# Kernel tuning notes

Hardware: AMD Instinct MI355X
Metric: run time of the kernel (lower is better)

The kernel has to match this reference:

```python
import jax, jax.numpy as jnp
import numpy as np
import math

M = 0.2
S = 30.0
COS_M = math.cos(M)
SIN_M = math.sin(M)
TH = math.cos(math.pi - M)
MM = math.sin(math.pi - M) * M


def setup_inputs() -> dict:
    key = jax.random.key(0)
    k1, k2, k3 = jax.random.split(key, 3)
    B, D, C = 1024, 192, 100000
    x = jax.random.normal(k1, (B, D), dtype=jnp.float32)
    weight = jax.random.normal(k2, (C, D), dtype=jnp.float32)
    label = jax.random.randint(k3, (B,), 0, C, dtype=jnp.int64)
    return {"x": x, "weight": weight, "label": label}


def _l2norm(v, axis=-1, eps=1e-12):
    # matches F.normalize(p=2): v / max(||v||, eps)
    n = jnp.sqrt(jnp.sum(v * v, axis=axis, keepdims=True))
    return v / jnp.maximum(n, eps)


def reference(x, weight, label):
    B = x.shape[0]
    cosine = _l2norm(x) @ _l2norm(weight).T            # [B, C]
    sine = jnp.sqrt(jnp.clip(1.0 - cosine * cosine, 0.0, 1.0))
    phi = cosine * COS_M - sine * SIN_M
    phi = jnp.where(cosine - TH > 0, phi, cosine - MM)
    one_hot = jax.nn.one_hot(label, cosine.shape[1], dtype=cosine.dtype)
    output = (one_hot * phi + (1.0 - one_hot) * cosine) * S
    # cross entropy (mean reduction)
    logp = jax.nn.log_softmax(output, axis=-1)
    loss = -jnp.mean(jnp.take_along_axis(logp, label[:, None], axis=1)[:, 0])
    # top-1 accuracy (percent), detached metric
    pred = jnp.argmax(output, axis=-1)
    prec1 = jnp.mean((pred == label).astype(jnp.float32)) * 100.0
    return loss, prec1
```

## Files before the change

### kernel.cpp

```cpp
#include <hip/hip_runtime.h>
#include <math.h>

#define B_ROWS   1024
#define DIM      192
#define NCLS     100000
#define S_SCALE  30.0f
#define COS_M    0.98006657784124163f
#define SIN_M    0.19866933079506122f
#define TH_C     (-0.98006657784124163f)
#define MM_C     0.039733866159012243f
#define L2E30    43.2808512266689f

#define NTILE_B  784
#define NCHUNKR  16
#define ASEG_CH  1536
#define NSLOT    1568

#define NCHUNKC  1568
#define CSPLIT   128
#define NSLOT2   128
#define PACK_WGRID 3136
#define PACK_GRID  3168

typedef float floatx4 __attribute__((ext_vector_type(4)));
typedef __bf16 bf16x8 __attribute__((ext_vector_type(8)));

__device__ __forceinline__ unsigned int f2bf(float x) {
    unsigned int u = __float_as_uint(x);
    u = (u + 0x7fffu + ((u >> 16) & 1u)) >> 16;
    return u;
}
__device__ __forceinline__ unsigned int pack2(float lo, float hi) {
    return f2bf(lo) | (f2bf(hi) << 16);
}
__device__ __forceinline__ float fexp2(float x) {
#if __has_builtin(__builtin_amdgcn_exp2f)
    return __builtin_amdgcn_exp2f(x);
#else
    float r; __asm__("v_exp_f32 %0, %1" : "=v"(r) : "v"(x)); return r;
#endif
}
template <int N>
__device__ __forceinline__ float ror16(float x) {
    return __int_as_float(__builtin_amdgcn_mov_dpp(
        __float_as_int(x), 0x120 | N, 0xF, 0xF, false));
}


__global__ __launch_bounds__(256)
void pack_kernel(const float* __restrict__ x, const float* __restrict__ w,
                 unsigned short* __restrict__ asw, unsigned short* __restrict__ wsw,
                 float* __restrict__ accum)
{
    const int bid = blockIdx.x;
    const int t = threadIdx.x;
    const int r = t >> 3, oct = t & 7;

    const float* src;
    unsigned short* dst;
    int row;
    bool live;
    if (bid < PACK_WGRID) {
        row = bid * 32 + r;  live = (row < NCLS);  src = w;  dst = wsw;
    } else {
        row = (bid - PACK_WGRID) * 32 + r;  live = true;  src = x;  dst = asw;
        if (bid == PACK_WGRID && t < 4) accum[t] = 0.0f;
    }

    float4 buf[6];
    float s = 0.f;
    if (live) {
        const float4* sp = (const float4*)(src + (size_t)row * DIM) + oct * 6;
        #pragma unroll
        for (int q = 0; q < 6; ++q) {
            float4 v = sp[q];
            buf[q] = v;
            s += v.x * v.x + v.y * v.y + v.z * v.z + v.w * v.w;
        }
    } else {
        #pragma unroll
        for (int q = 0; q < 6; ++q) buf[q] = make_float4(0.f, 0.f, 0.f, 0.f);
    }
    s += __shfl_xor(s, 1);
    s += __shfl_xor(s, 2);
    s += __shfl_xor(s, 4);
    const float inv = live ? (1.0f / fmaxf(sqrtf(s), 1e-12f)) : 0.0f;

    const int cc = row >> 6, c64 = row & 63;
    #pragma unroll
    for (int j = 0; j < 3; ++j) {
        const int k8 = oct * 3 + j;
        uint4 o;
        float4 a0 = buf[2 * j], a1 = buf[2 * j + 1];
        o.x = pack2(a0.x * inv, a0.y * inv);
        o.y = pack2(a0.z * inv, a0.w * inv);
        o.z = pack2(a1.x * inv, a1.y * inv);
        o.w = pack2(a1.z * inv, a1.w * inv);
        *(uint4*)(dst + ((size_t)(cc * 24 + k8) * 64 + c64) * 8) = o;
    }
}

__global__ __launch_bounds__(256, 2)
void gemm_stats4_kernel(const unsigned short* __restrict__ asw,
                        const unsigned short* __restrict__ wsw,
                        float2* __restrict__ pslot)
{
    const int bid  = blockIdx.x;
    const int cs   = bid & 127;
    const int rb   = bid >> 7;
    const int tid  = threadIdx.x;
    const int wv   = tid >> 6;
    const int lane = tid & 63;
    const int quad = lane >> 4, mrow = lane & 15;

    bf16x8 xfr[4][6];
    {
        const unsigned short* ab = asw + (size_t)(rb * 4 + wv) * (24 * 64 * 8);
        #pragma unroll
        for (int a = 0; a < 4; ++a)
            #pragma unroll
            for (int ks = 0; ks < 6; ++ks)
                xfr[a][ks] = *(const bf16x8*)(ab +
                    (size_t)((ks * 4 + quad) * 64 + a * 16 + mrow) * 8);
    }

    const int nch   = 12 + (cs < 32 ? 1 : 0);
    const int cbase = cs * 12 + (cs < 32 ? cs : 32);
    const unsigned short* wp = wsw + (size_t)cbase * 12288
                             + quad * 512 + mrow * 8;

    float s_acc[4][4];
    float m_acc[4][4];
    #pragma unroll
    for (int a = 0; a < 4; ++a)
        #pragma unroll
        for (int r = 0; r < 4; ++r) { s_acc[a][r] = 0.f; m_acc[a][r] = -1e30f; }

    bf16x8 b0[4], b1[4];
    #pragma unroll
    for (int ni = 0; ni < 4; ++ni) {
        b0[ni] = *(const bf16x8*)(wp + ni * 128);
        b1[ni] = *(const bf16x8*)(wp + 2048 + ni * 128);
    }

    #pragma unroll 1
    for (int c = 0; c < nch; ++c, wp += 12288) {
        floatx4 acc[4][4];
        #pragma unroll
        for (int a = 0; a < 4; ++a)
            #pragma unroll
            for (int ni = 0; ni < 4; ++ni) {
                floatx4 z = {0.f, 0.f, 0.f, 0.f};
                acc[a][ni] = z;
            }
        #pragma unroll
        for (int ks = 0; ks < 6; ++ks) {
            const unsigned short* np = wp + (size_t)(ks + 2) * 2048;
            bf16x8 n0 = *(const bf16x8*)(np);
            bf16x8 n1 = *(const bf16x8*)(np + 128);
            bf16x8 n2 = *(const bf16x8*)(np + 256);
            bf16x8 n3 = *(const bf16x8*)(np + 384);
            __builtin_amdgcn_s_setprio(1);
            #pragma unroll
            for (int a = 0; a < 4; ++a) {
                acc[a][0] = __builtin_amdgcn_mfma_f32_16x16x32_bf16(
                    xfr[a][ks], b0[0], acc[a][0], 0, 0, 0);
                acc[a][1] = __builtin_amdgcn_mfma_f32_16x16x32_bf16(
                    xfr[a][ks], b0[1], acc[a][1], 0, 0, 0);
                acc[a][2] = __builtin_amdgcn_mfma_f32_16x16x32_bf16(
                    xfr[a][ks], b0[2], acc[a][2], 0, 0, 0);
                acc[a][3] = __builtin_amdgcn_mfma_f32_16x16x32_bf16(
                    xfr[a][ks], b0[3], acc[a][3], 0, 0, 0);
            }
            __builtin_amdgcn_s_setprio(0);
            b0[0] = b1[0]; b0[1] = b1[1]; b0[2] = b1[2]; b0[3] = b1[3];
            b1[0] = n0;    b1[1] = n1;    b1[2] = n2;    b1[3] = n3;
        }
        #pragma unroll
        for (int a = 0; a < 4; ++a)
            #pragma unroll
            for (int r = 0; r < 4; ++r) {
                float v0 = acc[a][0][r], v1 = acc[a][1][r];
                float v2 = acc[a][2][r], v3 = acc[a][3][r];
                m_acc[a][r] = fmaxf(fmaxf(fmaxf(fmaxf(v0, v1), v2), v3),
                                    m_acc[a][r]);
                s_acc[a][r] += (fexp2(fmaf(v0, L2E30, -L2E30))
                              + fexp2(fmaf(v1, L2E30, -L2E30)))
                             + (fexp2(fmaf(v2, L2E30, -L2E30))
                              + fexp2(fmaf(v3, L2E30, -L2E30)));
            }
    }

    const int rowb = rb * 256 + wv * 64;
    #pragma unroll
    for (int a = 0; a < 4; ++a)
        #pragma unroll
        for (int r = 0; r < 4; ++r) {
            float s = s_acc[a][r], m = m_acc[a][r];
            s += ror16<1>(s); s += ror16<2>(s); s += ror16<4>(s); s += ror16<8>(s);
            m = fmaxf(m, ror16<1>(m)); m = fmaxf(m, ror16<2>(m));
            m = fmaxf(m, ror16<4>(m)); m = fmaxf(m, ror16<8>(m));
            if (mrow == 0)
                pslot[(size_t)cs * B_ROWS + rowb + a * 16 + quad * 4 + r] =
                    make_float2(m, s);
        }
}

__global__ __launch_bounds__(256)
void finalize2_kernel(const float2* __restrict__ pslot,
                      const float* __restrict__ x, const float* __restrict__ w,
                      const int* __restrict__ label,
                      float* __restrict__ accum, float* __restrict__ out)
{
    __shared__ float2 red[8][32];
    const int t = threadIdx.x, rr = t & 31, g = t >> 5;
    {
        const int row = blockIdx.x * 32 + rr;
        float M = -1e30f, L = 0.f;
        #pragma unroll
        for (int s = 0; s < NSLOT2 / 8; ++s) {
            float2 p = pslot[(size_t)(s * 8 + g) * B_ROWS + row];
            M = fmaxf(M, p.x);
            L += p.y;
        }
        red[g][rr] = make_float2(M, L);
    }
    __syncthreads();
    if (t < 32) {
        const int row = blockIdx.x * 32 + t;
        float Mc = -1e30f, L = 0.f;
        #pragma unroll
        for (int g2 = 0; g2 < 8; ++g2) {
            float2 p = red[g2][t];
            Mc = fmaxf(Mc, p.x);
            L += p.y;
        }

        const int lab = label[row];
        const float4* xr = (const float4*)(x + (size_t)row * DIM);
        const float4* wr = (const float4*)(w + (size_t)lab * DIM);
        float dot = 0.f, nx = 0.f, nw = 0.f;
        #pragma unroll
        for (int q = 0; q < 48; ++q) {
            float4 a = xr[q], b = wr[q];
            dot += a.x * b.x + a.y * b.y + a.z * b.z + a.w * b.w;
            nx  += a.x * a.x + a.y * a.y + a.z * a.z + a.w * a.w;
            nw  += b.x * b.x + b.y * b.y + b.z * b.z + b.w * b.w;
        }
        float cosl    = dot / fmaxf(sqrtf(nx) * sqrtf(nw), 1e-12f);
        float t_plain = S_SCALE * cosl;
        float sine    = sqrtf(fmaxf(0.f, fminf(1.f, 1.f - cosl * cosl)));
        float phi     = cosl * COS_M - sine * SIN_M;
        float modv    = ((cosl - TH_C) > 0.f) ? phi : (cosl - MM_C);
        float t_mod   = S_SCALE * modv;

        float Ladj = L - __expf(t_plain - 30.0f) + __expf(t_mod - 30.0f);
        Ladj = fmaxf(Ladj, 1e-37f);
        float loss = (30.0f + logf(Ladj)) - t_mod;
        float corr = (t_mod > S_SCALE * Mc) ? 1.f : 0.f;

        #pragma unroll
        for (int off = 16; off > 0; off >>= 1) {
            loss += __shfl_xor(loss, off);
            corr += __shfl_xor(corr, off);
        }
        if (t == 0) {
            atomicAdd(&accum[0], loss);
            atomicAdd(&accum[1], corr);
            __threadfence();
            int old = atomicAdd((int*)accum + 2, 1);
            if (old == (int)gridDim.x - 1) {
                float a0 = atomicAdd(&accum[0], 0.0f);
                float a1 = atomicAdd(&accum[1], 0.0f);
                out[0] = a0 * (1.0f / (float)B_ROWS);
                out[1] = a1 * (100.0f / (float)B_ROWS);
            }
        }
    }
}


__global__ __launch_bounds__(256)
void prep_kernel(const float* __restrict__ x, unsigned short* __restrict__ asw,
                 float* __restrict__ accum)
{
    const int ab = blockIdx.x;
    const int t = threadIdx.x;
    if (ab == 0 && t < 4) accum[t] = 0.0f;
    const int r = t >> 1, half = t & 1;
    const int row = ab * 128 + r;
    const int c = ab * 2 + (r >> 6);
    const int r64 = r & 63;

    float4 buf[24];
    float s = 0.f;
    const float4* sp = (const float4*)(x + (size_t)row * DIM) + half * 24;
    #pragma unroll
    for (int q = 0; q < 24; ++q) {
        float4 v = sp[q];
        buf[q] = v;
        s += v.x * v.x + v.y * v.y + v.z * v.z + v.w * v.w;
    }
    s += __shfl_xor(s, 1);
    const float inv = 1.0f / fmaxf(sqrtf(s), 1e-12f);
    #pragma unroll
    for (int j = 0; j < 12; ++j) {
        const int k8 = half * 12 + j;
        uint4 o;
        float4 a0 = buf[2 * j], a1 = buf[2 * j + 1];
        o.x = pack2(a0.x * inv, a0.y * inv);
        o.y = pack2(a0.z * inv, a0.w * inv);
        o.z = pack2(a1.x * inv, a1.y * inv);
        o.w = pack2(a1.z * inv, a1.w * inv);
        *(uint4*)(asw + ((size_t)c * ASEG_CH + k8 * 64 + r64) * 8) = o;
    }
}

__global__ __launch_bounds__(256, 3)
void gemm_stats_kernel(const float* __restrict__ w,
                       const unsigned short* __restrict__ asw,
                       unsigned int* __restrict__ pslot)
{
    __shared__ __align__(16) char lds[49152];
    const int tid  = threadIdx.x;
    const int wave = tid >> 6;
    const int lane = tid & 63;
    const int quad = lane >> 4;
    const int mrow = lane & 15;
    const int rg   = wave >> 1;
    const int cgr  = wave & 1;

    {
        const int r = tid >> 1, half = tid & 1;
        const int col = blockIdx.x * 128 + r;
        const bool live = (col < NCLS);
        float4 buf[24];
        float s = 0.f;
        if (live) {
            const float4* sp = (const float4*)(w + (size_t)col * DIM) + half * 24;
            #pragma unroll
            for (int q = 0; q < 24; ++q) {
                float4 v = sp[q];
                buf[q] = v;
                s += v.x * v.x + v.y * v.y + v.z * v.z + v.w * v.w;
            }
        }
        s += __shfl_xor(s, 1);
        const float inv = live ? (1.0f / fmaxf(sqrtf(s), 1e-12f)) : 0.0f;
        #pragma unroll
        for (int j = 0; j < 12; ++j) {
            const int k8 = half * 12 + j;
            uint4 o = make_uint4(0u, 0u, 0u, 0u);
            if (live) {
                float4 a0 = buf[2 * j], a1 = buf[2 * j + 1];
                o.x = pack2(a0.x * inv, a0.y * inv);
                o.y = pack2(a0.z * inv, a0.w * inv);
                o.z = pack2(a1.x * inv, a1.y * inv);
                o.w = pack2(a1.z * inv, a1.w * inv);
            }
            *(uint4*)(lds + (size_t)(k8 * 128 + r) * 16) = o;
        }
    }
    __syncthreads();

    bf16x8 bfr[6][4];
    #pragma unroll
    for (int ks = 0; ks < 6; ++ks)
        #pragma unroll
        for (int ni = 0; ni < 4; ++ni)
            bfr[ks][ni] = *(const bf16x8*)(lds +
                (((ks * 4 + quad) * 128) + cgr * 64 + ni * 16 + mrow) * 16);

    const int slot = blockIdx.x * 2 + cgr;
    #pragma unroll 2
    for (int c = 0; c < NCHUNKR; ++c) {
        const unsigned short* ab = asw + (size_t)c * ASEG_CH * 8;
        floatx4 acc[2][4];
        #pragma unroll
        for (int mi = 0; mi < 2; ++mi)
            #pragma unroll
            for (int ni = 0; ni < 4; ++ni) {
                floatx4 z = {0.f, 0.f, 0.f, 0.f};
                acc[mi][ni] = z;
            }
        #pragma unroll
        for (int ks = 0; ks < 6; ++ks) {
            bf16x8 a0 = *(const bf16x8*)(ab +
                (size_t)(((ks * 4 + quad) * 64) + rg * 32 + mrow) * 8);
            bf16x8 a1 = *(const bf16x8*)(ab +
                (size_t)(((ks * 4 + quad) * 64) + rg * 32 + 16 + mrow) * 8);
            #pragma unroll
            for (int ni = 0; ni < 4; ++ni)
                acc[0][ni] = __builtin_amdgcn_mfma_f32_16x16x32_bf16(
                    a0, bfr[ks][ni], acc[0][ni], 0, 0, 0);
            #pragma unroll
            for (int ni = 0; ni < 4; ++ni)
                acc[1][ni] = __builtin_amdgcn_mfma_f32_16x16x32_bf16(
                    a1, bfr[ks][ni], acc[1][ni], 0, 0, 0);
        }

        #pragma unroll
        for (int mi = 0; mi < 2; ++mi)
            #pragma unroll
            for (int r = 0; r < 4; ++r) {
                float v0 = acc[mi][0][r], v1 = acc[mi][1][r];
                float v2 = acc[mi][2][r], v3 = acc[mi][3][r];
                float m = fmaxf(fmaxf(v0, v1), fmaxf(v2, v3));
                float s = fexp2(fmaf(v0, L2E30, -L2E30))
                        + fexp2(fmaf(v1, L2E30, -L2E30))
                        + fexp2(fmaf(v2, L2E30, -L2E30))
                        + fexp2(fmaf(v3, L2E30, -L2E30));
                s += ror16<1>(s); s += ror16<2>(s);
                s += ror16<4>(s); s += ror16<8>(s);
                m = fmaxf(m, ror16<1>(m)); m = fmaxf(m, ror16<2>(m));
                m = fmaxf(m, ror16<4>(m)); m = fmaxf(m, ror16<8>(m));
                if (mrow == mi * 4 + r)
                    pslot[(size_t)slot * B_ROWS +
                          c * 64 + rg * 32 + mi * 16 + quad * 4 + r] = pack2(m, s);
            }
    }
}

__global__ __launch_bounds__(256)
void finalize_kernel(const unsigned int* __restrict__ pslot,
                     const float* __restrict__ x, const float* __restrict__ w,
                     const int* __restrict__ label,
                     float* __restrict__ accum, float* __restrict__ out)
{
    __shared__ float2 red[8][32];
    const int t = threadIdx.x, rr = t & 31, g = t >> 5;
    {
        const int row = blockIdx.x * 32 + rr;
        float M = -1e30f, L = 0.f;
        for (int s = g; s < NSLOT; s += 8) {
            unsigned int u = pslot[(size_t)s * B_ROWS + row];
            M = fmaxf(M, __uint_as_float(u << 16));
            L += __uint_as_float(u & 0xFFFF0000u);
        }
        red[g][rr] = make_float2(M, L);
    }
    __syncthreads();
    if (t < 32) {
        const int row = blockIdx.x * 32 + t;
        float Mc = -1e30f, L = 0.f;
        #pragma unroll
        for (int g2 = 0; g2 < 8; ++g2) {
            float2 p = red[g2][t];
            Mc = fmaxf(Mc, p.x);
            L += p.y;
        }

        const int lab = label[row];
        const float4* xr = (const float4*)(x + (size_t)row * DIM);
        const float4* wr = (const float4*)(w + (size_t)lab * DIM);
        float dot = 0.f, nx = 0.f, nw = 0.f;
        #pragma unroll
        for (int q = 0; q < 48; ++q) {
            float4 a = xr[q], b = wr[q];
            dot += a.x * b.x + a.y * b.y + a.z * b.z + a.w * b.w;
            nx  += a.x * a.x + a.y * a.y + a.z * a.z + a.w * a.w;
            nw  += b.x * b.x + b.y * b.y + b.z * b.z + b.w * b.w;
        }
        float cosl    = dot / fmaxf(sqrtf(nx) * sqrtf(nw), 1e-12f);
        float t_plain = S_SCALE * cosl;
        float sine    = sqrtf(fmaxf(0.f, fminf(1.f, 1.f - cosl * cosl)));
        float phi     = cosl * COS_M - sine * SIN_M;
        float modv    = ((cosl - TH_C) > 0.f) ? phi : (cosl - MM_C);
        float t_mod   = S_SCALE * modv;

        float Ladj = L - __expf(t_plain - 30.0f) + __expf(t_mod - 30.0f);
        Ladj = fmaxf(Ladj, 1e-37f);
        float loss = (30.0f + logf(Ladj)) - t_mod;
        float corr = (t_mod > S_SCALE * Mc) ? 1.f : 0.f;

        #pragma unroll
        for (int off = 16; off > 0; off >>= 1) {
            loss += __shfl_xor(loss, off);
            corr += __shfl_xor(corr, off);
        }
        if (t == 0) {
            atomicAdd(&accum[0], loss);
            atomicAdd(&accum[1], corr);
            __threadfence();
            int old = atomicAdd((int*)accum + 2, 1);
            if (old == (int)gridDim.x - 1) {
                float a0 = atomicAdd(&accum[0], 0.0f);
                float a1 = atomicAdd(&accum[1], 0.0f);
                out[0] = a0 * (1.0f / (float)B_ROWS);
                out[1] = a1 * (100.0f / (float)B_ROWS);
            }
        }
    }
}

extern "C" void kernel_launch(void* const* d_in, const int* in_sizes, int n_in,
                              void* d_out, int out_size, void* d_ws, size_t ws_size,
                              hipStream_t stream)
{
    const float* x     = (const float*)d_in[0];
    const float* w     = (const float*)d_in[1];
    const int*   label = (const int*)d_in[2];
    float* out = (float*)d_out;

    char* ws = (char*)d_ws;
    float* accum = (float*)ws;
    unsigned short* asw = (unsigned short*)(ws + 256);
    const size_t asw_bytes = (size_t)NCHUNKR * ASEG_CH * 16;

    const size_t wsw_bytes    = (size_t)NCHUNKC * 24 * 64 * 16;
    const size_t pslot2_bytes = (size_t)NSLOT2 * B_ROWS * 8;
    const size_t need_new = 256 + asw_bytes + wsw_bytes + pslot2_bytes;

    if (ws_size >= need_new) {
        unsigned short* wsw = (unsigned short*)(ws + 256 + asw_bytes);
        float2* pslot2 = (float2*)(ws + 256 + asw_bytes + wsw_bytes);
        pack_kernel<<<dim3(PACK_GRID), dim3(256), 0, stream>>>(x, w, asw, wsw, accum);
        gemm_stats4_kernel<<<dim3(4 * CSPLIT), dim3(256), 0, stream>>>(asw, wsw, pslot2);
        finalize2_kernel<<<dim3(B_ROWS / 32), dim3(256), 0, stream>>>(
            pslot2, x, w, label, accum, out);
    } else {
        unsigned int* pslot = (unsigned int*)(ws + 256 + asw_bytes);
        prep_kernel<<<dim3(8), dim3(256), 0, stream>>>(x, asw, accum);
        gemm_stats_kernel<<<dim3(NTILE_B), dim3(256), 0, stream>>>(w, asw, pslot);
        finalize_kernel<<<dim3(B_ROWS / 32), dim3(256), 0, stream>>>(
            pslot, x, w, label, accum, out);
    }
}
```

Baseline: 168.5 us.

## Switch GEMM to 32x32x16 MFMA and fold log2e*30 scale into packed x

Replaces the 16x16x32 MFMA tiling with 32x32x16 MFMAs over two 32-row tiles per wave, with a 4-deep rotating register prefetch of weight fragments. The softmax scale (30*log2e) is folded into the x normalization during packing, so the epilogue feeds accumulators straight into exp2 and drops the per-element FMA. Finalize rescales the sum by exp(-30) and converts the max back from log2 units. Folding the scale into bf16 x changes rounding slightly, and without the -30 offset the exp2 sums may get large, though they stay within fp32 range.

```diff
diff --git a/kernel.cpp b/kernel.cpp
--- a/kernel.cpp
+++ b/kernel.cpp
@@ -10,6 +10,8 @@
 #define TH_C     (-0.98006657784124163f)
 #define MM_C     0.039733866159012243f
 #define L2E30    43.2808512266689f
+#define EXPM30   9.357622968840175e-14f
+#define LN2_C    0.69314718055994531f
 
 #define NTILE_B  784
 #define NCHUNKR  16
@@ -22,7 +24,8 @@
 #define PACK_WGRID 3136
 #define PACK_GRID  3168
 
-typedef float floatx4 __attribute__((ext_vector_type(4)));
+typedef float floatx4  __attribute__((ext_vector_type(4)));
+typedef float floatx16 __attribute__((ext_vector_type(16)));
 typedef __bf16 bf16x8 __attribute__((ext_vector_type(8)));
 
 __device__ __forceinline__ unsigned int f2bf(float x) {
@@ -60,10 +63,11 @@
     unsigned short* dst;
     int row;
     bool live;
+    bool isx;
     if (bid < PACK_WGRID) {
-        row = bid * 32 + r;  live = (row < NCLS);  src = w;  dst = wsw;
+        row = bid * 32 + r;  live = (row < NCLS);  src = w;  dst = wsw;  isx = false;
     } else {
-        row = (bid - PACK_WGRID) * 32 + r;  live = true;  src = x;  dst = asw;
+        row = (bid - PACK_WGRID) * 32 + r;  live = true;  src = x;  dst = asw;  isx = true;
         if (bid == PACK_WGRID && t < 4) accum[t] = 0.0f;
     }
 
@@ -84,7 +88,8 @@
     s += __shfl_xor(s, 1);
     s += __shfl_xor(s, 2);
     s += __shfl_xor(s, 4);
-    const float inv = live ? (1.0f / fmaxf(sqrtf(s), 1e-12f)) : 0.0f;
+    float inv = live ? (1.0f / fmaxf(sqrtf(s), 1e-12f)) : 0.0f;
+    if (isx) inv *= L2E30;
 
     const int cc = row >> 6, c64 = row & 63;
     #pragma unroll
@@ -100,8 +105,14 @@
     }
 }
 
+__device__ __forceinline__ constexpr int poff(int q) {
+    return (q < 12) ? q * 1024
+         : (q < 24) ? 256 + (q - 12) * 1024
+                    : 12288 + (q - 24) * 1024;
+}
+
 __global__ __launch_bounds__(256, 2)
-void gemm_stats4_kernel(const unsigned short* __restrict__ asw,
+void gemm_stats5_kernel(const unsigned short* __restrict__ asw,
                         const unsigned short* __restrict__ wsw,
                         float2* __restrict__ pslot)
 {
@@ -111,98 +122,91 @@
     const int tid  = threadIdx.x;
     const int wv   = tid >> 6;
     const int lane = tid & 63;
-    const int quad = lane >> 4, mrow = lane & 15;
-
-    bf16x8 xfr[4][6];
+    const int col  = lane & 31;
+    const int kh   = lane >> 5;
+
+    bf16x8 xfr[2][12];
     {
-        const unsigned short* ab = asw + (size_t)(rb * 4 + wv) * (24 * 64 * 8);
-        #pragma unroll
-        for (int a = 0; a < 4; ++a)
+        const unsigned short* al = asw + (size_t)(rb * 4 + wv) * 12288
+                                 + kh * 512 + col * 8;
+        #pragma unroll
+        for (int t = 0; t < 2; ++t)
             #pragma unroll
-            for (int ks = 0; ks < 6; ++ks)
-                xfr[a][ks] = *(const bf16x8*)(ab +
-                    (size_t)((ks * 4 + quad) * 64 + a * 16 + mrow) * 8);
+            for (int ks = 0; ks < 12; ++ks)
+                xfr[t][ks] = *(const bf16x8*)(al + ks * 1024 + t * 256);
     }
 
     const int nch   = 12 + (cs < 32 ? 1 : 0);
     const int cbase = cs * 12 + (cs < 32 ? cs : 32);
     const unsigned short* wp = wsw + (size_t)cbase * 12288
-                             + quad * 512 + mrow * 8;
-
-    float s_acc[4][4];
-    float m_acc[4][4];
-    #pragma unroll
-    for (int a = 0; a < 4; ++a)
-        #pragma unroll
-        for (int r = 0; r < 4; ++r) { s_acc[a][r] = 0.f; m_acc[a][r] = -1e30f; }
-
-    bf16x8 b0[4], b1[4];
-    #pragma unroll
-    for (int ni = 0; ni < 4; ++ni) {
-        b0[ni] = *(const bf16x8*)(wp + ni * 128);
-        b1[ni] = *(const bf16x8*)(wp + 2048 + ni * 128);
-    }
+                             + kh * 512 + col * 8;
+
+    float s_acc[2][16];
+    float m_acc[2][16];
+    #pragma unroll
+    for (int t = 0; t < 2; ++t)
+        #pragma unroll
+        for (int r = 0; r < 16; ++r) { s_acc[t][r] = 0.f; m_acc[t][r] = -1e30f; }
+
+    bf16x8 bL[4];
+    #pragma unroll
+    for (int i = 0; i < 4; ++i)
+        bL[i] = *(const bf16x8*)(wp + poff(i));
 
     #pragma unroll 1
     for (int c = 0; c < nch; ++c, wp += 12288) {
-        floatx4 acc[4][4];
-        #pragma unroll
-        for (int a = 0; a < 4; ++a)
-            #pragma unroll
-            for (int ni = 0; ni < 4; ++ni) {
-                floatx4 z = {0.f, 0.f, 0.f, 0.f};
-                acc[a][ni] = z;
-            }
-        #pragma unroll
-        for (int ks = 0; ks < 6; ++ks) {
-            const unsigned short* np = wp + (size_t)(ks + 2) * 2048;
-            bf16x8 n0 = *(const bf16x8*)(np);
-            bf16x8 n1 = *(const bf16x8*)(np + 128);
-            bf16x8 n2 = *(const bf16x8*)(np + 256);
-            bf16x8 n3 = *(const bf16x8*)(np + 384);
-            __builtin_amdgcn_s_setprio(1);
-            #pragma unroll
-            for (int a = 0; a < 4; ++a) {
-                acc[a][0] = __builtin_amdgcn_mfma_f32_16x16x32_bf16(
-                    xfr[a][ks], b0[0], acc[a][0], 0, 0, 0);
-                acc[a][1] = __builtin_amdgcn_mfma_f32_16x16x32_bf16(
-                    xfr[a][ks], b0[1], acc[a][1], 0, 0, 0);
-                acc[a][2] = __builtin_amdgcn_mfma_f32_16x16x32_bf16(
-                    xfr[a][ks], b0[2], acc[a][2], 0, 0, 0);
-                acc[a][3] = __builtin_amdgcn_mfma_f32_16x16x32_bf16(
-                    xfr[a][ks], b0[3], acc[a][3], 0, 0, 0);
-            }
-            __builtin_amdgcn_s_setprio(0);
-            b0[0] = b1[0]; b0[1] = b1[1]; b0[2] = b1[2]; b0[3] = b1[3];
-            b1[0] = n0;    b1[1] = n1;    b1[2] = n2;    b1[3] = n3;
-        }
-        #pragma unroll
-        for (int a = 0; a < 4; ++a)
-            #pragma unroll
-            for (int r = 0; r < 4; ++r) {
-                float v0 = acc[a][0][r], v1 = acc[a][1][r];
-                float v2 = acc[a][2][r], v3 = acc[a][3][r];
-                m_acc[a][r] = fmaxf(fmaxf(fmaxf(fmaxf(v0, v1), v2), v3),
-                                    m_acc[a][r]);
-                s_acc[a][r] += (fexp2(fmaf(v0, L2E30, -L2E30))
-                              + fexp2(fmaf(v1, L2E30, -L2E30)))
-                             + (fexp2(fmaf(v2, L2E30, -L2E30))
-                              + fexp2(fmaf(v3, L2E30, -L2E30)));
-            }
+        floatx16 accA, accB;
+        #pragma unroll
+        for (int r = 0; r < 16; ++r) { accA[r] = 0.f; accB[r] = 0.f; }
+        #pragma unroll
+        for (int p = 0; p < 12; ++p) {
+            bf16x8 bf = bL[p & 3];
+            bL[p & 3] = *(const bf16x8*)(wp + poff(p + 4));
+            accA = __builtin_amdgcn_mfma_f32_32x32x16_bf16(xfr[0][p], bf, accA, 0, 0, 0);
+            accB = __builtin_amdgcn_mfma_f32_32x32x16_bf16(xfr[1][p], bf, accB, 0, 0, 0);
+        }
+        #pragma unroll
+        for (int r = 0; r < 16; ++r) {
+            float vA = accA[r], vB = accB[r];
+            m_acc[0][r] = fmaxf(m_acc[0][r], vA);
+            m_acc[1][r] = fmaxf(m_acc[1][r], vB);
+            s_acc[0][r] += fexp2(vA);
+            s_acc[1][r] += fexp2(vB);
+        }
+        #pragma unroll
+        for (int r = 0; r < 16; ++r) { accA[r] = 0.f; accB[r] = 0.f; }
+        #pragma unroll
+        for (int p = 12; p < 24; ++p) {
+            bf16x8 bf = bL[p & 3];
+            bL[p & 3] = *(const bf16x8*)(wp + poff(p + 4));
+            accA = __builtin_amdgcn_mfma_f32_32x32x16_bf16(xfr[0][p - 12], bf, accA, 0, 0, 0);
+            accB = __builtin_amdgcn_mfma_f32_32x32x16_bf16(xfr[1][p - 12], bf, accB, 0, 0, 0);
+        }
+        #pragma unroll
+        for (int r = 0; r < 16; ++r) {
+            float vA = accA[r], vB = accB[r];
+            m_acc[0][r] = fmaxf(m_acc[0][r], vA);
+            m_acc[1][r] = fmaxf(m_acc[1][r], vB);
+            s_acc[0][r] += fexp2(vA);
+            s_acc[1][r] += fexp2(vB);
+        }
     }
 
     const int rowb = rb * 256 + wv * 64;
     #pragma unroll
-    for (int a = 0; a < 4; ++a)
-        #pragma unroll
-        for (int r = 0; r < 4; ++r) {
-            float s = s_acc[a][r], m = m_acc[a][r];
+    for (int t = 0; t < 2; ++t)
+        #pragma unroll
+        for (int r = 0; r < 16; ++r) {
+            float s = s_acc[t][r], m = m_acc[t][r];
             s += ror16<1>(s); s += ror16<2>(s); s += ror16<4>(s); s += ror16<8>(s);
+            s += __shfl_xor(s, 16);
             m = fmaxf(m, ror16<1>(m)); m = fmaxf(m, ror16<2>(m));
             m = fmaxf(m, ror16<4>(m)); m = fmaxf(m, ror16<8>(m));
-            if (mrow == 0)
-                pslot[(size_t)cs * B_ROWS + rowb + a * 16 + quad * 4 + r] =
-                    make_float2(m, s);
+            m = fmaxf(m, __shfl_xor(m, 16));
+            if (col == 0) {
+                const int rl = (r & 3) + 8 * (r >> 2) + 4 * kh + t * 32;
+                pslot[(size_t)cs * B_ROWS + rowb + rl] = make_float2(m, s);
+            }
         }
 }
 
@@ -254,10 +258,10 @@
         float modv    = ((cosl - TH_C) > 0.f) ? phi : (cosl - MM_C);
         float t_mod   = S_SCALE * modv;
 
-        float Ladj = L - __expf(t_plain - 30.0f) + __expf(t_mod - 30.0f);
+        float Ladj = L * EXPM30 - __expf(t_plain - 30.0f) + __expf(t_mod - 30.0f);
         Ladj = fmaxf(Ladj, 1e-37f);
         float loss = (30.0f + logf(Ladj)) - t_mod;
-        float corr = (t_mod > S_SCALE * Mc) ? 1.f : 0.f;
+        float corr = (t_mod > Mc * LN2_C) ? 1.f : 0.f;
 
         #pragma unroll
         for (int off = 16; off > 0; off >>= 1) {
@@ -515,7 +519,7 @@
         unsigned short* wsw = (unsigned short*)(ws + 256 + asw_bytes);
         float2* pslot2 = (float2*)(ws + 256 + asw_bytes + wsw_bytes);
         pack_kernel<<<dim3(PACK_GRID), dim3(256), 0, stream>>>(x, w, asw, wsw, accum);
-        gemm_stats4_kernel<<<dim3(4 * CSPLIT), dim3(256), 0, stream>>>(asw, wsw, pslot2);
+        gemm_stats5_kernel<<<dim3(4 * CSPLIT), dim3(256), 0, stream>>>(asw, wsw, pslot2);
         finalize2_kernel<<<dim3(B_ROWS / 32), dim3(256), 0, stream>>>(
             pslot2, x, w, label, accum, out);
     } else {
```

Result: slower. 174.7 us (+3.7%).

## Stage weight tiles through double-buffered LDS and fold exp scale into packed activations

Applied to the files above, without the earlier changes.

The GEMM kernel now loads each weight chunk into a double-buffered LDS region with a register-staged prefetch of the next chunk, replacing the per-wave direct global register double buffer. The pack kernel writes through LDS for coalesced stores, reorders its block-to-chunk mapping to follow the GEMM consumer order, and pre-multiplies normalized x by log2(e)*30 so the softmax exp needs no per-element FMA. Finalize rescales the sum and the max comparison to match. This adds a barrier per chunk and LDS traffic, and increases bf16 rounding exposure on the scaled activations.

```diff
diff --git a/kernel.cpp b/kernel.cpp
--- a/kernel.cpp
+++ b/kernel.cpp
@@ -10,6 +10,8 @@
 #define TH_C     (-0.98006657784124163f)
 #define MM_C     0.039733866159012243f
 #define L2E30    43.2808512266689f
+#define EXPM30   9.357622968840175e-14f
+#define LN2_C    0.69314718055994531f
 
 #define NTILE_B  784
 #define NCHUNKR  16
@@ -48,25 +50,43 @@
 
 
 __global__ __launch_bounds__(256)
-void pack_kernel(const float* __restrict__ x, const float* __restrict__ w,
-                 unsigned short* __restrict__ asw, unsigned short* __restrict__ wsw,
-                 float* __restrict__ accum)
-{
+void pack2_kernel(const float* __restrict__ x, const float* __restrict__ w,
+                  unsigned short* __restrict__ asw, unsigned short* __restrict__ wsw,
+                  float* __restrict__ accum)
+{
+    __shared__ uint4 lds_pk[32][25];
     const int bid = blockIdx.x;
     const int t = threadIdx.x;
     const int r = t >> 3, oct = t & 7;
 
     const float* src;
-    unsigned short* dst;
-    int row;
-    bool live;
+    unsigned short* dstc;
+    int rowbase, half;
+    bool wside;
     if (bid < PACK_WGRID) {
-        row = bid * 32 + r;  live = (row < NCLS);  src = w;  dst = wsw;
+        const int k = bid & 7, j = bid >> 3;
+        int cs, cc, h;
+        if (j < 104) {
+            const int i = j / 26; h = j % 26;
+            cs = k + 8 * i;  cc = cs * 13 + (h >> 1);
+        } else {
+            const int j2 = j - 104;
+            const int i = 4 + j2 / 24; h = j2 % 24;
+            cs = k + 8 * i;  cc = 416 + (cs - 32) * 12 + (h >> 1);
+        }
+        half = h & 1;
+        rowbase = cc * 64 + half * 32;
+        src = w;  dstc = wsw + (size_t)cc * 12288;  wside = true;
     } else {
-        row = (bid - PACK_WGRID) * 32 + r;  live = true;  src = x;  dst = asw;
+        const int xb = bid - PACK_WGRID;
+        half = xb & 1;
+        rowbase = xb * 32;
+        src = x;  dstc = asw + (size_t)(xb >> 1) * 12288;  wside = false;
         if (bid == PACK_WGRID && t < 4) accum[t] = 0.0f;
     }
 
+    const int row = rowbase + r;
+    const bool live = !wside || (row < NCLS);
     float4 buf[6];
     float s = 0.f;
     if (live) {
@@ -84,9 +104,9 @@
     s += __shfl_xor(s, 1);
     s += __shfl_xor(s, 2);
     s += __shfl_xor(s, 4);
-    const float inv = live ? (1.0f / fmaxf(sqrtf(s), 1e-12f)) : 0.0f;
-
-    const int cc = row >> 6, c64 = row & 63;
+    float inv = live ? (1.0f / fmaxf(sqrtf(s), 1e-12f)) : 0.0f;
+    if (!wside) inv *= L2E30;
+
     #pragma unroll
     for (int j = 0; j < 3; ++j) {
         const int k8 = oct * 3 + j;
@@ -96,15 +116,24 @@
         o.y = pack2(a0.z * inv, a0.w * inv);
         o.z = pack2(a1.x * inv, a1.y * inv);
         o.w = pack2(a1.z * inv, a1.w * inv);
-        *(uint4*)(dst + ((size_t)(cc * 24 + k8) * 64 + c64) * 8) = o;
+        lds_pk[r][k8] = o;
+    }
+    __syncthreads();
+    #pragma unroll
+    for (int j = 0; j < 3; ++j) {
+        const int flat = j * 256 + t;
+        const int sseg = flat >> 5, rr = flat & 31;
+        *(uint4*)(dstc + ((size_t)(sseg * 64) + half * 32 + rr) * 8)
+            = lds_pk[rr][sseg];
     }
 }
 
 __global__ __launch_bounds__(256, 2)
-void gemm_stats4_kernel(const unsigned short* __restrict__ asw,
+void gemm_stats7_kernel(const unsigned short* __restrict__ asw,
                         const unsigned short* __restrict__ wsw,
                         float2* __restrict__ pslot)
 {
+    __shared__ __align__(16) char lds[49152];
     const int bid  = blockIdx.x;
     const int cs   = bid & 127;
     const int rb   = bid >> 7;
@@ -115,7 +144,7 @@
 
     bf16x8 xfr[4][6];
     {
-        const unsigned short* ab = asw + (size_t)(rb * 4 + wv) * (24 * 64 * 8);
+        const unsigned short* ab = asw + (size_t)(rb * 4 + wv) * 12288;
         #pragma unroll
         for (int a = 0; a < 4; ++a)
             #pragma unroll
@@ -124,10 +153,9 @@
                     (size_t)((ks * 4 + quad) * 64 + a * 16 + mrow) * 8);
     }
 
-    const int nch   = 12 + (cs < 32 ? 1 : 0);
-    const int cbase = cs * 12 + (cs < 32 ? cs : 32);
-    const unsigned short* wp = wsw + (size_t)cbase * 12288
-                             + quad * 512 + mrow * 8;
+    const int nch = 12 + (cs < 32 ? 1 : 0);
+    const char* wp0 = (const char*)(wsw
+                    + (size_t)(cs * 12 + (cs < 32 ? cs : 32)) * 12288);
 
     float s_acc[4][4];
     float m_acc[4][4];
@@ -136,15 +164,32 @@
         #pragma unroll
         for (int r = 0; r < 4; ++r) { s_acc[a][r] = 0.f; m_acc[a][r] = -1e30f; }
 
-    bf16x8 b0[4], b1[4];
-    #pragma unroll
-    for (int ni = 0; ni < 4; ++ni) {
-        b0[ni] = *(const bf16x8*)(wp + ni * 128);
-        b1[ni] = *(const bf16x8*)(wp + 2048 + ni * 128);
-    }
+    const int soff = wv * 6144 + lane * 16;
+    uint4 st[6];
+
+    {
+        const char* g = wp0 + soff;
+        #pragma unroll
+        for (int i = 0; i < 6; ++i)
+            st[i] = *(const uint4*)(g + i * 1024);
+        char* l = lds + soff;
+        #pragma unroll
+        for (int i = 0; i < 6; ++i)
+            *(uint4*)(l + i * 1024) = st[i];
+    }
+    __syncthreads();
 
     #pragma unroll 1
-    for (int c = 0; c < nch; ++c, wp += 12288) {
+    for (int c = 0; c < nch; ++c) {
+        const bool more = (c + 1 < nch);
+        if (more) {
+            const char* g = wp0 + (size_t)(c + 1) * 24576 + soff;
+            #pragma unroll
+            for (int i = 0; i < 6; ++i)
+                st[i] = *(const uint4*)(g + i * 1024);
+        }
+
+        const char* bb = lds + (c & 1) * 24576;
         floatx4 acc[4][4];
         #pragma unroll
         for (int a = 0; a < 4; ++a)
@@ -155,26 +200,22 @@
             }
         #pragma unroll
         for (int ks = 0; ks < 6; ++ks) {
-            const unsigned short* np = wp + (size_t)(ks + 2) * 2048;
-            bf16x8 n0 = *(const bf16x8*)(np);
-            bf16x8 n1 = *(const bf16x8*)(np + 128);
-            bf16x8 n2 = *(const bf16x8*)(np + 256);
-            bf16x8 n3 = *(const bf16x8*)(np + 384);
-            __builtin_amdgcn_s_setprio(1);
+            const char* sb = bb + (size_t)((ks * 4 + quad) * 64 + mrow) * 16;
+            bf16x8 b0 = *(const bf16x8*)(sb);
+            bf16x8 b1 = *(const bf16x8*)(sb + 256);
+            bf16x8 b2 = *(const bf16x8*)(sb + 512);
+            bf16x8 b3 = *(const bf16x8*)(sb + 768);
             #pragma unroll
             for (int a = 0; a < 4; ++a) {
                 acc[a][0] = __builtin_amdgcn_mfma_f32_16x16x32_bf16(
-                    xfr[a][ks], b0[0], acc[a][0], 0, 0, 0);
+                    xfr[a][ks], b0, acc[a][0], 0, 0, 0);
                 acc[a][1] = __builtin_amdgcn_mfma_f32_16x16x32_bf16(
-                    xfr[a][ks], b0[1], acc[a][1], 0, 0, 0);
+                    xfr[a][ks], b1, acc[a][1], 0, 0, 0);
                 acc[a][2] = __builtin_amdgcn_mfma_f32_16x16x32_bf16(
-                    xfr[a][ks], b0[2], acc[a][2], 0, 0, 0);
+                    xfr[a][ks], b2, acc[a][2], 0, 0, 0);
                 acc[a][3] = __builtin_amdgcn_mfma_f32_16x16x32_bf16(
-                    xfr[a][ks], b0[3], acc[a][3], 0, 0, 0);
-            }
-            __builtin_amdgcn_s_setprio(0);
-            b0[0] = b1[0]; b0[1] = b1[1]; b0[2] = b1[2]; b0[3] = b1[3];
-            b1[0] = n0;    b1[1] = n1;    b1[2] = n2;    b1[3] = n3;
+                    xfr[a][ks], b3, acc[a][3], 0, 0, 0);
+            }
         }
         #pragma unroll
         for (int a = 0; a < 4; ++a)
@@ -184,11 +225,16 @@
                 float v2 = acc[a][2][r], v3 = acc[a][3][r];
                 m_acc[a][r] = fmaxf(fmaxf(fmaxf(fmaxf(v0, v1), v2), v3),
                                     m_acc[a][r]);
-                s_acc[a][r] += (fexp2(fmaf(v0, L2E30, -L2E30))
-                              + fexp2(fmaf(v1, L2E30, -L2E30)))
-                             + (fexp2(fmaf(v2, L2E30, -L2E30))
-                              + fexp2(fmaf(v3, L2E30, -L2E30)));
-            }
+                s_acc[a][r] += (fexp2(v0) + fexp2(v1))
+                             + (fexp2(v2) + fexp2(v3));
+            }
+        if (more) {
+            char* l = lds + ((c + 1) & 1) * 24576 + soff;
+            #pragma unroll
+            for (int i = 0; i < 6; ++i)
+                *(uint4*)(l + i * 1024) = st[i];
+        }
+        __syncthreads();
     }
 
     const int rowb = rb * 256 + wv * 64;
@@ -254,10 +300,10 @@
         float modv    = ((cosl - TH_C) > 0.f) ? phi : (cosl - MM_C);
         float t_mod   = S_SCALE * modv;
 
-        float Ladj = L - __expf(t_plain - 30.0f) + __expf(t_mod - 30.0f);
+        float Ladj = L * EXPM30 - __expf(t_plain - 30.0f) + __expf(t_mod - 30.0f);
         Ladj = fmaxf(Ladj, 1e-37f);
         float loss = (30.0f + logf(Ladj)) - t_mod;
-        float corr = (t_mod > S_SCALE * Mc) ? 1.f : 0.f;
+        float corr = (t_mod > Mc * LN2_C) ? 1.f : 0.f;
 
         #pragma unroll
         for (int off = 16; off > 0; off >>= 1) {
@@ -514,8 +560,8 @@
     if (ws_size >= need_new) {
         unsigned short* wsw = (unsigned short*)(ws + 256 + asw_bytes);
         float2* pslot2 = (float2*)(ws + 256 + asw_bytes + wsw_bytes);
-        pack_kernel<<<dim3(PACK_GRID), dim3(256), 0, stream>>>(x, w, asw, wsw, accum);
-        gemm_stats4_kernel<<<dim3(4 * CSPLIT), dim3(256), 0, stream>>>(asw, wsw, pslot2);
+        pack2_kernel<<<dim3(PACK_GRID), dim3(256), 0, stream>>>(x, w, asw, wsw, accum);
+        gemm_stats7_kernel<<<dim3(4 * CSPLIT), dim3(256), 0, stream>>>(asw, wsw, pslot2);
         finalize2_kernel<<<dim3(B_ROWS / 32), dim3(256), 0, stream>>>(
             pslot2, x, w, label, accum, out);
     } else {
```

Measured after the change: 177.9 us. 1.06x slower.
